# Kernel tuning notes

Measured on AMD Instinct MI355X. Metric: run time of the kernel, lower is better.

Reference implementation:

```python
import jax, jax.numpy as jnp
import numpy as np

N, DIM, H, HD = 2048, 1280, 16, 80

def _rotate_half(x):
    x1, x2 = x[..., :x.shape[-1] // 2], x[..., x.shape[-1] // 2:]
    return jnp.concatenate((-x2, x1), axis=-1)

def setup_inputs() -> dict:
    key = jax.random.key(0)
    ks = jax.random.split(key, 6)
    hidden_states = jax.random.normal(ks[0], (N, DIM), dtype=jnp.float32)
    cu_seqlens = jnp.array([0, N // 2, N], dtype=jnp.int32)  # 2 packed segments
    # rotary embeddings: half-dim inverse frequencies, duplicated to head_dim
    inv_freq = 1.0 / (10000.0 ** (np.arange(0, HD // 2, dtype=np.float32) * 2.0 / HD))
    pos = np.arange(N, dtype=np.float32) % (N // 2)  # positions restart per segment
    freqs = pos[:, None] * inv_freq[None, :]           # [N, HD/2]
    emb = jnp.asarray(np.concatenate([freqs, freqs], axis=-1))  # [N, HD]
    cos, sin = jnp.cos(emb), jnp.sin(emb)
    Wqkv = jax.random.normal(ks[1], (DIM, 3 * DIM), dtype=jnp.float32) * (DIM ** -0.5)
    bqkv = jax.random.normal(ks[2], (3 * DIM,), dtype=jnp.float32) * 0.02
    Wproj = jax.random.normal(ks[3], (DIM, DIM), dtype=jnp.float32) * (DIM ** -0.5)
    bproj = jax.random.normal(ks[4], (DIM,), dtype=jnp.float32) * 0.02
    return {"hidden_states": hidden_states, "cu_seqlens": cu_seqlens,
            "cos": cos, "sin": sin, "Wqkv": Wqkv, "bqkv": bqkv,
            "Wproj": Wproj, "bproj": bproj}

def reference(hidden_states, cu_seqlens, cos, sin, Wqkv, bqkv, Wproj, bproj):
    n = hidden_states.shape[0]
    scale = HD ** -0.5
    qkv = (hidden_states @ Wqkv + bqkv).reshape(n, 3, H, HD)
    q, k, v = qkv[:, 0], qkv[:, 1], qkv[:, 2]           # each [N, H, HD]
    # RoPE (fp32), cos/sin broadcast over heads: [N, 1, HD]
    c, s = cos[:, None, :], sin[:, None, :]
    q = q * c + _rotate_half(q) * s
    k = k * c + _rotate_half(k) * s
    # block-diagonal varlen mask from cu_seqlens (per-segment full attention)
    seg_id = jnp.searchsorted(cu_seqlens, jnp.arange(n), side='right')  # [N]
    mask = seg_id[:, None] == seg_id[None, :]                           # [N, N]
    scores = jnp.einsum('qhd,khd->hqk', q, k) * scale                   # [H, N, N]
    scores = jnp.where(mask[None], scores, -jnp.inf)
    attn = jax.nn.softmax(scores.astype(jnp.float32), axis=-1).astype(q.dtype)
    out = jnp.einsum('hqk,khd->qhd', attn, v).reshape(n, H * HD)        # [N, DIM]
    return out @ Wproj + bproj
```

## Files before the change

### kernel.cpp

```cpp
#include <hip/hip_runtime.h>
#include <hip/hip_bf16.h>

constexpr int N_TOK  = 2048;
constexpr int DIM    = 1280;
constexpr int NHEAD  = 16;
constexpr int HD     = 80;
constexpr int QKV_N  = 3 * DIM;

using bf16 = __hip_bfloat16;
typedef __attribute__((ext_vector_type(4))) float f32x4;
typedef __attribute__((ext_vector_type(8))) short short8;

__device__ __forceinline__ float b2f(bf16 x) { return __bfloat162float(x); }
__device__ __forceinline__ bf16  f2b(float x) { return __float2bfloat16(x); }

typedef const __attribute__((address_space(1))) unsigned int* gas_u32;
typedef __attribute__((address_space(3))) unsigned int* las_u32;
__device__ __forceinline__ void gload_lds16(const void* g, void* l) {
  __builtin_amdgcn_global_load_lds((gas_u32)g, (las_u32)l, 16, 0, 0);
}

__device__ __forceinline__ void transpose_body(const float* __restrict__ W,
                                               bf16* __restrict__ WT, int K, int N) {
  __shared__ float tile[32][33];
  const int n0 = blockIdx.x * 32, k0 = blockIdx.y * 32;
  const int tc = threadIdx.x & 31, tr = threadIdx.x >> 5;
#pragma unroll
  for (int r = tr; r < 32; r += 8)
    tile[r][tc] = W[(size_t)(k0 + r) * N + n0 + tc];
  __syncthreads();
#pragma unroll
  for (int r = tr; r < 32; r += 8)
    WT[(size_t)(n0 + r) * K + k0 + tc] = f2b(tile[tc][r]);
}

__global__ __launch_bounds__(256)
void prep_kernel(const float* __restrict__ hs, bf16* __restrict__ hsb,
                 const float* __restrict__ Wqkv, bf16* __restrict__ WqkvT,
                 const float* __restrict__ Wproj, bf16* __restrict__ WprojT) {
  if (blockIdx.z == 0) {
    const int bid = blockIdx.y * gridDim.x + blockIdx.x;
    if (bid >= (N_TOK * DIM) / 2048) return;
    const int i = bid * 2048 + threadIdx.x * 8;
    const float4 a = *reinterpret_cast<const float4*>(hs + i);
    const float4 b = *reinterpret_cast<const float4*>(hs + i + 4);
    __align__(16) bf16 w[8] = {f2b(a.x), f2b(a.y), f2b(a.z), f2b(a.w),
                               f2b(b.x), f2b(b.y), f2b(b.z), f2b(b.w)};
    *reinterpret_cast<short8*>(hsb + i) = *reinterpret_cast<const short8*>(w);
  } else if (blockIdx.z == 1) {
    transpose_body(Wqkv, WqkvT, DIM, QKV_N);
  } else {
    if (blockIdx.x >= DIM / 32) return;
    transpose_body(Wproj, WprojT, DIM, DIM);
  }
}

template <int OBF>
__global__ __launch_bounds__(256)
void mfma_gemm(const bf16* __restrict__ A, const bf16* __restrict__ BT,
               const float* __restrict__ bias, void* __restrict__ C,
               int M, int N, int K) {
  __shared__ bf16 As[128 * 64];
  __shared__ bf16 Bs[128 * 64];
  const int tid = threadIdx.x;
  const int wid = tid >> 6, lane = tid & 63;
  const int lm = lane & 15, kg = lane >> 4;
  const int wm = (wid >> 1) * 64, wn = (wid & 1) * 64;
  const int m0 = blockIdx.y * 128, n0 = blockIdx.x * 128;

  const int srow = lane >> 3;
  const int sblk = (lane & 7) ^ srow;

  f32x4 acc[4][4];
#pragma unroll
  for (int i = 0; i < 4; ++i)
#pragma unroll
    for (int j = 0; j < 4; ++j) acc[i][j] = (f32x4){0.f, 0.f, 0.f, 0.f};

  for (int k0 = 0; k0 < K; k0 += 64) {
#pragma unroll
    for (int i = 0; i < 4; ++i) {
      const int slot = i * 4 + wid;
      const int row = slot * 8 + srow;
      gload_lds16(A + (size_t)(m0 + row) * K + k0 + sblk * 8, &As[slot * 512]);
      gload_lds16(BT + (size_t)(n0 + row) * K + k0 + sblk * 8, &Bs[slot * 512]);
    }
    __syncthreads();

#pragma unroll
    for (int kh = 0; kh < 2; ++kh) {
      short8 af[4], bfr[4];
#pragma unroll
      for (int t = 0; t < 4; ++t) {
        const int ar = wm + t * 16 + lm;
        af[t] = *reinterpret_cast<const short8*>(
            &As[ar * 64 + ((kh * 4 + kg) ^ (ar & 7)) * 8]);
        const int br = wn + t * 16 + lm;
        bfr[t] = *reinterpret_cast<const short8*>(
            &Bs[br * 64 + ((kh * 4 + kg) ^ (br & 7)) * 8]);
      }
#pragma unroll
      for (int mi = 0; mi < 4; ++mi)
#pragma unroll
        for (int ni = 0; ni < 4; ++ni)
          acc[mi][ni] = __builtin_amdgcn_mfma_f32_16x16x32_bf16(
              af[mi], bfr[ni], acc[mi][ni], 0, 0, 0);
    }
    __syncthreads();
  }

#pragma unroll
  for (int mi = 0; mi < 4; ++mi) {
#pragma unroll
    for (int ni = 0; ni < 4; ++ni) {
      const int col = n0 + wn + ni * 16 + lm;
      const float bv = bias[col];
#pragma unroll
      for (int r = 0; r < 4; ++r) {
        const int row = m0 + wm + mi * 16 + kg * 4 + r;
        const float v = acc[mi][ni][r] + bv;
        if constexpr (OBF)
          ((bf16*)C)[(size_t)row * N + col] = f2b(v);
        else
          ((float*)C)[(size_t)row * N + col] = v;
      }
    }
  }
}

__global__ void rope_kernel(bf16* __restrict__ qkv, const float* __restrict__ cosb,
                            const float* __restrict__ sinb) {
  constexpr int HALF = HD / 2;
  int idx = blockIdx.x * blockDim.x + threadIdx.x;
  int n     = idx / (2 * NHEAD * HALF);
  int rem   = idx % (2 * NHEAD * HALF);
  int which = rem / (NHEAD * HALF);
  int rem2  = rem % (NHEAD * HALF);
  int h     = rem2 / HALF;
  int d     = rem2 % HALF;
  size_t base = (size_t)n * QKV_N + which * DIM + h * HD;
  float x1 = b2f(qkv[base + d]), x2 = b2f(qkv[base + d + HALF]);
  float c1 = cosb[n * HD + d], c2 = cosb[n * HD + d + HALF];
  float s1 = sinb[n * HD + d], s2 = sinb[n * HD + d + HALF];
  qkv[base + d]        = f2b(x1 * c1 - x2 * s1);
  qkv[base + d + HALF] = f2b(x2 * c2 + x1 * s2);
}

constexpr int KC   = 64;
constexpr int KSTR = 104;
constexpr int VSTR = 88;
constexpr int PSTR = 72;

__global__ __launch_bounds__(512)
void attn_mfma_kernel(const bf16* __restrict__ qkv, const int* __restrict__ cu,
                      bf16* __restrict__ out, int nseg) {
  __shared__ bf16 Ks[2][KC * KSTR];
  __shared__ bf16 Vt[HD * VSTR];
  __shared__ bf16 Pl[8 * 16 * PSTR];

  const int p = blockIdx.x;
  const int lidx = (p & 7) * (gridDim.x >> 3) + (p >> 3);
  const int xt  = lidx & 15;
  const int seg = (lidx >> 4) % nseg;
  const int h   = (lidx >> 4) / nseg;

  const int s0 = cu[seg], s1 = cu[seg + 1];
  if (s0 + xt * 128 >= s1) return;

  const int tid  = threadIdx.x;
  const int wid  = tid >> 6, lane = tid & 63;
  const int lm = lane & 15, kg = lane >> 4;
  const int qrow = s0 + xt * 128 + wid * 16 + lm;
  const float scale = 0.11180339887498949f;

  if (tid < 384) {
    int b = tid / 192, rem = tid % 192, r = rem / 3, sl = rem % 3;
    *reinterpret_cast<short8*>(&Ks[b][r * KSTR + 80 + sl * 8]) =
        (short8){0, 0, 0, 0, 0, 0, 0, 0};
  }

  short8 qa[3];
#pragma unroll
  for (int ck = 0; ck < 3; ++ck) {
    const int dbase = ck * 32 + kg * 8;
    if (qrow < s1 && dbase < HD)
      qa[ck] = *reinterpret_cast<const short8*>(
          qkv + (size_t)qrow * QKV_N + h * HD + dbase);
    else
      qa[ck] = (short8){0, 0, 0, 0, 0, 0, 0, 0};
  }

  short8 kreg[2], vreg[4];
  const int vgrp = tid / 10, vsl = tid % 10;
  auto issueK = [&](int c) {
    const int k0 = s0 + c * KC;
    {
      const int r = min(k0 + tid / 10, s1 - 1);
      kreg[0] = *reinterpret_cast<const short8*>(
          qkv + (size_t)r * QKV_N + DIM + h * HD + (tid % 10) * 8);
    }
    if (tid < 128) {
      const int s = tid + 512;
      const int r = min(k0 + s / 10, s1 - 1);
      kreg[1] = *reinterpret_cast<const short8*>(
          qkv + (size_t)r * QKV_N + DIM + h * HD + (s % 10) * 8);
    }
  };
  auto commitK = [&](int buf) {
    *reinterpret_cast<short8*>(&Ks[buf][(tid / 10) * KSTR + (tid % 10) * 8]) =
        kreg[0];
    if (tid < 128) {
      const int s = tid + 512;
      *reinterpret_cast<short8*>(&Ks[buf][(s / 10) * KSTR + (s % 10) * 8]) =
          kreg[1];
    }
  };
  auto issueV = [&](int c) {
    if (tid < 160) {
      const int k0 = s0 + c * KC;
#pragma unroll
      for (int e = 0; e < 4; ++e) {
        const int r = min(k0 + vgrp * 4 + e, s1 - 1);
        vreg[e] = *reinterpret_cast<const short8*>(
            qkv + (size_t)r * QKV_N + 2 * DIM + h * HD + vsl * 8);
      }
    }
  };
  auto commitV = [&]() {
    if (tid < 160) {
      const int r0 = vgrp * 4;
      const int swz = (vsl & 7) << 3;
#pragma unroll
      for (int de = 0; de < 8; ++de) {
        __align__(8) bf16 w[4] = {reinterpret_cast<const bf16*>(&vreg[0])[de],
                                  reinterpret_cast<const bf16*>(&vreg[1])[de],
                                  reinterpret_cast<const bf16*>(&vreg[2])[de],
                                  reinterpret_cast<const bf16*>(&vreg[3])[de]};
        *reinterpret_cast<uint2*>(&Vt[(vsl * 8 + de) * VSTR + (r0 ^ swz)]) =
            *reinterpret_cast<const uint2*>(w);
      }
    }
  };

  f32x4 oacc[5];
#pragma unroll
  for (int dt = 0; dt < 5; ++dt) oacc[dt] = (f32x4){0.f, 0.f, 0.f, 0.f};
  float m = -1e30f, l = 0.f;
  const int plbase = (wid * 16 + lm) * PSTR;
  const int nch = (s1 - s0 + KC - 1) / KC;

  issueK(0);
  issueV(0);
  commitK(0);
  if (nch > 1) issueK(1);
  __syncthreads();

  for (int c = 0; c < nch; ++c) {
    const int cur = c & 1;
    const int nk = min(KC, s1 - (s0 + c * KC));

    commitV();

    f32x4 sc[4];
    __builtin_amdgcn_s_setprio(1);
#pragma unroll
    for (int mi = 0; mi < 4; ++mi) {
      sc[mi] = (f32x4){0.f, 0.f, 0.f, 0.f};
#pragma unroll
      for (int ck = 0; ck < 3; ++ck) {
        short8 ka = *reinterpret_cast<const short8*>(
            &Ks[cur][(mi * 16 + lm) * KSTR + ck * 32 + kg * 8]);
        sc[mi] = __builtin_amdgcn_mfma_f32_16x16x32_bf16(ka, qa[ck], sc[mi], 0, 0, 0);
      }
    }
    __builtin_amdgcn_s_setprio(0);

    if (c + 1 < nch) {
      commitK(cur ^ 1);
      issueV(c + 1);
    }
    if (c + 2 < nch) issueK(c + 2);

#pragma unroll
    for (int mi = 0; mi < 4; ++mi) sc[mi] *= scale;
    if (nk < KC) {
#pragma unroll
      for (int mi = 0; mi < 4; ++mi)
#pragma unroll
        for (int r = 0; r < 4; ++r)
          if (mi * 16 + kg * 4 + r >= nk) sc[mi][r] = -1e30f;
    }
    f32x4 m4 = sc[0];
#pragma unroll
    for (int mi = 1; mi < 4; ++mi) {
      m4[0] = fmaxf(m4[0], sc[mi][0]); m4[1] = fmaxf(m4[1], sc[mi][1]);
      m4[2] = fmaxf(m4[2], sc[mi][2]); m4[3] = fmaxf(m4[3], sc[mi][3]);
    }
    const float rml = fmaxf(fmaxf(m4[0], m4[1]), fmaxf(m4[2], m4[3]));
    if (!__all(rml - m <= 8.0f)) {
      float rm = rml;
      rm = fmaxf(rm, __shfl_xor(rm, 16));
      rm = fmaxf(rm, __shfl_xor(rm, 32));
      const float mnew = fmaxf(m, rm);
      const float fs = __expf(m - mnew);
      m = mnew;
      l *= fs;
#pragma unroll
      for (int dt = 0; dt < 5; ++dt) oacc[dt] *= fs;
    }
    f32x4 pp[4];
#pragma unroll
    for (int mi = 0; mi < 4; ++mi) {
#pragma unroll
      for (int r = 0; r < 4; ++r) {
        pp[mi][r] = __expf(sc[mi][r] - m);
        l += pp[mi][r];
      }
    }
#pragma unroll
    for (int mi = 0; mi < 4; ++mi) {
      __align__(8) bf16 w[4] = {f2b(pp[mi][0]), f2b(pp[mi][1]),
                                f2b(pp[mi][2]), f2b(pp[mi][3])};
      *reinterpret_cast<uint2*>(&Pl[plbase + mi * 16 + kg * 4]) =
          *reinterpret_cast<const uint2*>(w);
    }

    __syncthreads();

    __builtin_amdgcn_s_setprio(1);
#pragma unroll
    for (int kc = 0; kc < 2; ++kc) {
      short8 pb = *reinterpret_cast<const short8*>(&Pl[plbase + kc * 32 + kg * 8]);
#pragma unroll
      for (int dt = 0; dt < 5; ++dt) {
        const int d = dt * 16 + lm;
        short8 va = *reinterpret_cast<const short8*>(
            &Vt[d * VSTR + ((kc * 32 + kg * 8) ^ (((d >> 3) & 7) << 3))]);
        oacc[dt] = __builtin_amdgcn_mfma_f32_16x16x32_bf16(va, pb, oacc[dt], 0, 0, 0);
      }
    }
    __builtin_amdgcn_s_setprio(0);

    __syncthreads();
  }

  l += __shfl_xor(l, 16);
  l += __shfl_xor(l, 32);
  if (qrow < s1) {
    const float inv = 1.f / l;
    bf16* op = out + (size_t)qrow * DIM + h * HD;
#pragma unroll
    for (int dt = 0; dt < 5; ++dt) {
      __align__(8) bf16 w[4] = {f2b(oacc[dt][0] * inv), f2b(oacc[dt][1] * inv),
                                f2b(oacc[dt][2] * inv), f2b(oacc[dt][3] * inv)};
      *reinterpret_cast<uint2*>(op + dt * 16 + kg * 4) =
          *reinterpret_cast<const uint2*>(w);
    }
  }
}

extern "C" void kernel_launch(void* const* d_in, const int* in_sizes, int n_in,
                              void* d_out, int out_size, void* d_ws, size_t ws_size,
                              hipStream_t stream) {
  const float* hs    = (const float*)d_in[0];
  const int*   cu    = (const int*)d_in[1];
  const float* cosb  = (const float*)d_in[2];
  const float* sinb  = (const float*)d_in[3];
  const float* Wqkv  = (const float*)d_in[4];
  const float* bqkv  = (const float*)d_in[5];
  const float* Wproj = (const float*)d_in[6];
  const float* bproj = (const float*)d_in[7];

  bf16* qkv      = (bf16*)d_ws;
  bf16* attn_out = qkv + (size_t)N_TOK * QKV_N;
  bf16* WqkvT    = attn_out + (size_t)N_TOK * DIM;
  bf16* WprojT   = WqkvT + (size_t)QKV_N * DIM;
  bf16* hsb      = WprojT + (size_t)DIM * DIM;

  prep_kernel<<<dim3(QKV_N / 32, DIM / 32, 3), 256, 0, stream>>>(
      hs, hsb, Wqkv, WqkvT, Wproj, WprojT);

  mfma_gemm<1><<<dim3(QKV_N / 128, N_TOK / 128), 256, 0, stream>>>(
      hsb, WqkvT, bqkv, qkv, N_TOK, QKV_N, DIM);

  rope_kernel<<<(N_TOK * 2 * NHEAD * (HD / 2)) / 256, 256, 0, stream>>>(
      qkv, cosb, sinb);

  int nseg = in_sizes[1] - 1;
  int nblk = (N_TOK / 128) * nseg * NHEAD;
  attn_mfma_kernel<<<nblk, 512, 0, stream>>>(qkv, cu, attn_out, nseg);

  mfma_gemm<0><<<dim3(DIM / 128, N_TOK / 128), 256, 0, stream>>>(
      attn_out, WprojT, bproj, d_out, N_TOK, DIM, DIM);
}
```

Baseline: 124.2 us.

## Process two query tiles per wave in attention to reuse K/V LDS fragments

The attention kernel now runs 256 threads (4 waves) per block instead of 512, and each wave handles 32 query rows as two 16-row MFMA tiles. Each K fragment and each V fragment read from LDS feeds two MFMAs, which halves LDS read traffic per unit of math and doubles the independent MFMA work in flight per wave. Online-softmax state (max, sum, output accumulators) is kept separately for each tile, and the K load and LDS padding loops are restructured for the smaller thread count. The cost is higher register pressure from the doubled accumulators, and fewer waves per block, which gives less latency hiding per block.

```diff
diff --git a/kernel.cpp b/kernel.cpp
--- a/kernel.cpp
+++ b/kernel.cpp
@@ -151,12 +151,12 @@
 constexpr int VSTR = 88;
 constexpr int PSTR = 72;
 
-__global__ __launch_bounds__(512)
+__global__ __launch_bounds__(256)
 void attn_mfma_kernel(const bf16* __restrict__ qkv, const int* __restrict__ cu,
                       bf16* __restrict__ out, int nseg) {
   __shared__ bf16 Ks[2][KC * KSTR];
   __shared__ bf16 Vt[HD * VSTR];
-  __shared__ bf16 Pl[8 * 16 * PSTR];
+  __shared__ bf16 Pl[128 * PSTR];
 
   const int p = blockIdx.x;
   const int lidx = (p & 7) * (gridDim.x >> 3) + (p >> 3);
@@ -170,49 +170,54 @@
   const int tid  = threadIdx.x;
   const int wid  = tid >> 6, lane = tid & 63;
   const int lm = lane & 15, kg = lane >> 4;
-  const int qrow = s0 + xt * 128 + wid * 16 + lm;
   const float scale = 0.11180339887498949f;
 
-  if (tid < 384) {
-    int b = tid / 192, rem = tid % 192, r = rem / 3, sl = rem % 3;
-    *reinterpret_cast<short8*>(&Ks[b][r * KSTR + 80 + sl * 8]) =
-        (short8){0, 0, 0, 0, 0, 0, 0, 0};
-  }
-
-  short8 qa[3];
+  const int qbase = s0 + xt * 128 + wid * 32 + lm;
+  const int qrow0 = qbase, qrow1 = qbase + 16;
+
+#pragma unroll
+  for (int t = 0; t < 2; ++t) {
+    const int s = tid + t * 256;
+    if (s < 384) {
+      int b = s / 192, rem = s % 192, r = rem / 3, sl = rem % 3;
+      *reinterpret_cast<short8*>(&Ks[b][r * KSTR + 80 + sl * 8]) =
+          (short8){0, 0, 0, 0, 0, 0, 0, 0};
+    }
+  }
+
+  short8 qa[3][2];
 #pragma unroll
   for (int ck = 0; ck < 3; ++ck) {
     const int dbase = ck * 32 + kg * 8;
-    if (qrow < s1 && dbase < HD)
-      qa[ck] = *reinterpret_cast<const short8*>(
-          qkv + (size_t)qrow * QKV_N + h * HD + dbase);
-    else
-      qa[ck] = (short8){0, 0, 0, 0, 0, 0, 0, 0};
-  }
-
-  short8 kreg[2], vreg[4];
+    qa[ck][0] = (qrow0 < s1 && dbase < HD)
+        ? *reinterpret_cast<const short8*>(qkv + (size_t)qrow0 * QKV_N + h * HD + dbase)
+        : (short8){0, 0, 0, 0, 0, 0, 0, 0};
+    qa[ck][1] = (qrow1 < s1 && dbase < HD)
+        ? *reinterpret_cast<const short8*>(qkv + (size_t)qrow1 * QKV_N + h * HD + dbase)
+        : (short8){0, 0, 0, 0, 0, 0, 0, 0};
+  }
+
+  short8 kreg[3], vreg[4];
   const int vgrp = tid / 10, vsl = tid % 10;
   auto issueK = [&](int c) {
     const int k0 = s0 + c * KC;
-    {
-      const int r = min(k0 + tid / 10, s1 - 1);
-      kreg[0] = *reinterpret_cast<const short8*>(
-          qkv + (size_t)r * QKV_N + DIM + h * HD + (tid % 10) * 8);
-    }
-    if (tid < 128) {
-      const int s = tid + 512;
-      const int r = min(k0 + s / 10, s1 - 1);
-      kreg[1] = *reinterpret_cast<const short8*>(
-          qkv + (size_t)r * QKV_N + DIM + h * HD + (s % 10) * 8);
+#pragma unroll
+    for (int t = 0; t < 3; ++t) {
+      const int s = tid + t * 256;
+      if (s < 640) {
+        const int r = min(k0 + s / 10, s1 - 1);
+        kreg[t] = *reinterpret_cast<const short8*>(
+            qkv + (size_t)r * QKV_N + DIM + h * HD + (s % 10) * 8);
+      }
     }
   };
   auto commitK = [&](int buf) {
-    *reinterpret_cast<short8*>(&Ks[buf][(tid / 10) * KSTR + (tid % 10) * 8]) =
-        kreg[0];
-    if (tid < 128) {
-      const int s = tid + 512;
-      *reinterpret_cast<short8*>(&Ks[buf][(s / 10) * KSTR + (s % 10) * 8]) =
-          kreg[1];
+#pragma unroll
+    for (int t = 0; t < 3; ++t) {
+      const int s = tid + t * 256;
+      if (s < 640)
+        *reinterpret_cast<short8*>(&Ks[buf][(s / 10) * KSTR + (s % 10) * 8]) =
+            kreg[t];
     }
   };
   auto issueV = [&](int c) {
@@ -242,11 +247,16 @@
     }
   };
 
-  f32x4 oacc[5];
-#pragma unroll
-  for (int dt = 0; dt < 5; ++dt) oacc[dt] = (f32x4){0.f, 0.f, 0.f, 0.f};
-  float m = -1e30f, l = 0.f;
-  const int plbase = (wid * 16 + lm) * PSTR;
+  f32x4 oacc[5][2];
+#pragma unroll
+  for (int dt = 0; dt < 5; ++dt) {
+    oacc[dt][0] = (f32x4){0.f, 0.f, 0.f, 0.f};
+    oacc[dt][1] = (f32x4){0.f, 0.f, 0.f, 0.f};
+  }
+  float m0v = -1e30f, m1v = -1e30f;
+  float l0 = 0.f, l1 = 0.f;
+  const int prow0 = (wid * 32 + lm) * PSTR;
+  const int prow1 = (wid * 32 + 16 + lm) * PSTR;
   const int nch = (s1 - s0 + KC - 1) / KC;
 
   issueK(0);
@@ -261,16 +271,20 @@
 
     commitV();
 
-    f32x4 sc[4];
+    f32x4 sc[4][2];
     __builtin_amdgcn_s_setprio(1);
 #pragma unroll
     for (int mi = 0; mi < 4; ++mi) {
-      sc[mi] = (f32x4){0.f, 0.f, 0.f, 0.f};
+      sc[mi][0] = (f32x4){0.f, 0.f, 0.f, 0.f};
+      sc[mi][1] = (f32x4){0.f, 0.f, 0.f, 0.f};
 #pragma unroll
       for (int ck = 0; ck < 3; ++ck) {
         short8 ka = *reinterpret_cast<const short8*>(
             &Ks[cur][(mi * 16 + lm) * KSTR + ck * 32 + kg * 8]);
-        sc[mi] = __builtin_amdgcn_mfma_f32_16x16x32_bf16(ka, qa[ck], sc[mi], 0, 0, 0);
+        sc[mi][0] = __builtin_amdgcn_mfma_f32_16x16x32_bf16(ka, qa[ck][0],
+                                                            sc[mi][0], 0, 0, 0);
+        sc[mi][1] = __builtin_amdgcn_mfma_f32_16x16x32_bf16(ka, qa[ck][1],
+                                                            sc[mi][1], 0, 0, 0);
       }
     }
     __builtin_amdgcn_s_setprio(0);
@@ -282,47 +296,66 @@
     if (c + 2 < nch) issueK(c + 2);
 
 #pragma unroll
-    for (int mi = 0; mi < 4; ++mi) sc[mi] *= scale;
+    for (int mi = 0; mi < 4; ++mi) {
+      sc[mi][0] *= scale;
+      sc[mi][1] *= scale;
+    }
     if (nk < KC) {
 #pragma unroll
       for (int mi = 0; mi < 4; ++mi)
 #pragma unroll
         for (int r = 0; r < 4; ++r)
-          if (mi * 16 + kg * 4 + r >= nk) sc[mi][r] = -1e30f;
-    }
-    f32x4 m4 = sc[0];
-#pragma unroll
-    for (int mi = 1; mi < 4; ++mi) {
-      m4[0] = fmaxf(m4[0], sc[mi][0]); m4[1] = fmaxf(m4[1], sc[mi][1]);
-      m4[2] = fmaxf(m4[2], sc[mi][2]); m4[3] = fmaxf(m4[3], sc[mi][3]);
-    }
-    const float rml = fmaxf(fmaxf(m4[0], m4[1]), fmaxf(m4[2], m4[3]));
-    if (!__all(rml - m <= 8.0f)) {
-      float rm = rml;
-      rm = fmaxf(rm, __shfl_xor(rm, 16));
-      rm = fmaxf(rm, __shfl_xor(rm, 32));
-      const float mnew = fmaxf(m, rm);
-      const float fs = __expf(m - mnew);
-      m = mnew;
-      l *= fs;
-#pragma unroll
-      for (int dt = 0; dt < 5; ++dt) oacc[dt] *= fs;
-    }
-    f32x4 pp[4];
+          if (mi * 16 + kg * 4 + r >= nk) {
+            sc[mi][0][r] = -1e30f;
+            sc[mi][1][r] = -1e30f;
+          }
+    }
+    float rml0 = sc[0][0][0], rml1 = sc[0][1][0];
+#pragma unroll
+    for (int mi = 0; mi < 4; ++mi)
+#pragma unroll
+      for (int r = 0; r < 4; ++r) {
+        if (mi | r) {
+          rml0 = fmaxf(rml0, sc[mi][0][r]);
+          rml1 = fmaxf(rml1, sc[mi][1][r]);
+        }
+      }
+    if (!__all(fmaxf(rml0 - m0v, rml1 - m1v) <= 8.0f)) {
+      float rm0 = rml0, rm1 = rml1;
+      rm0 = fmaxf(rm0, __shfl_xor(rm0, 16));
+      rm0 = fmaxf(rm0, __shfl_xor(rm0, 32));
+      rm1 = fmaxf(rm1, __shfl_xor(rm1, 16));
+      rm1 = fmaxf(rm1, __shfl_xor(rm1, 32));
+      const float mn0 = fmaxf(m0v, rm0), mn1 = fmaxf(m1v, rm1);
+      const float fs0 = __expf(m0v - mn0), fs1 = __expf(m1v - mn1);
+      m0v = mn0; m1v = mn1;
+      l0 *= fs0; l1 *= fs1;
+#pragma unroll
+      for (int dt = 0; dt < 5; ++dt) {
+        oacc[dt][0] *= fs0;
+        oacc[dt][1] *= fs1;
+      }
+    }
 #pragma unroll
     for (int mi = 0; mi < 4; ++mi) {
 #pragma unroll
       for (int r = 0; r < 4; ++r) {
-        pp[mi][r] = __expf(sc[mi][r] - m);
-        l += pp[mi][r];
+        sc[mi][0][r] = __expf(sc[mi][0][r] - m0v);
+        l0 += sc[mi][0][r];
+        sc[mi][1][r] = __expf(sc[mi][1][r] - m1v);
+        l1 += sc[mi][1][r];
       }
     }
 #pragma unroll
     for (int mi = 0; mi < 4; ++mi) {
-      __align__(8) bf16 w[4] = {f2b(pp[mi][0]), f2b(pp[mi][1]),
-                                f2b(pp[mi][2]), f2b(pp[mi][3])};
-      *reinterpret_cast<uint2*>(&Pl[plbase + mi * 16 + kg * 4]) =
-          *reinterpret_cast<const uint2*>(w);
+      __align__(8) bf16 w0[4] = {f2b(sc[mi][0][0]), f2b(sc[mi][0][1]),
+                                 f2b(sc[mi][0][2]), f2b(sc[mi][0][3])};
+      __align__(8) bf16 w1[4] = {f2b(sc[mi][1][0]), f2b(sc[mi][1][1]),
+                                 f2b(sc[mi][1][2]), f2b(sc[mi][1][3])};
+      *reinterpret_cast<uint2*>(&Pl[prow0 + mi * 16 + kg * 4]) =
+          *reinterpret_cast<const uint2*>(w0);
+      *reinterpret_cast<uint2*>(&Pl[prow1 + mi * 16 + kg * 4]) =
+          *reinterpret_cast<const uint2*>(w1);
     }
 
     __syncthreads();
@@ -330,13 +363,17 @@
     __builtin_amdgcn_s_setprio(1);
 #pragma unroll
     for (int kc = 0; kc < 2; ++kc) {
-      short8 pb = *reinterpret_cast<const short8*>(&Pl[plbase + kc * 32 + kg * 8]);
+      short8 pb0 = *reinterpret_cast<const short8*>(&Pl[prow0 + kc * 32 + kg * 8]);
+      short8 pb1 = *reinterpret_cast<const short8*>(&Pl[prow1 + kc * 32 + kg * 8]);
 #pragma unroll
       for (int dt = 0; dt < 5; ++dt) {
         const int d = dt * 16 + lm;
         short8 va = *reinterpret_cast<const short8*>(
             &Vt[d * VSTR + ((kc * 32 + kg * 8) ^ (((d >> 3) & 7) << 3))]);
-        oacc[dt] = __builtin_amdgcn_mfma_f32_16x16x32_bf16(va, pb, oacc[dt], 0, 0, 0);
+        oacc[dt][0] = __builtin_amdgcn_mfma_f32_16x16x32_bf16(va, pb0,
+                                                              oacc[dt][0], 0, 0, 0);
+        oacc[dt][1] = __builtin_amdgcn_mfma_f32_16x16x32_bf16(va, pb1,
+                                                              oacc[dt][1], 0, 0, 0);
       }
     }
     __builtin_amdgcn_s_setprio(0);
@@ -344,15 +381,28 @@
     __syncthreads();
   }
 
-  l += __shfl_xor(l, 16);
-  l += __shfl_xor(l, 32);
-  if (qrow < s1) {
-    const float inv = 1.f / l;
-    bf16* op = out + (size_t)qrow * DIM + h * HD;
+  l0 += __shfl_xor(l0, 16);
+  l0 += __shfl_xor(l0, 32);
+  l1 += __shfl_xor(l1, 16);
+  l1 += __shfl_xor(l1, 32);
+  if (qrow0 < s1) {
+    const float inv = 1.f / l0;
+    bf16* op = out + (size_t)qrow0 * DIM + h * HD;
 #pragma unroll
     for (int dt = 0; dt < 5; ++dt) {
-      __align__(8) bf16 w[4] = {f2b(oacc[dt][0] * inv), f2b(oacc[dt][1] * inv),
-                                f2b(oacc[dt][2] * inv), f2b(oacc[dt][3] * inv)};
+      __align__(8) bf16 w[4] = {f2b(oacc[dt][0][0] * inv), f2b(oacc[dt][0][1] * inv),
+                                f2b(oacc[dt][0][2] * inv), f2b(oacc[dt][0][3] * inv)};
+      *reinterpret_cast<uint2*>(op + dt * 16 + kg * 4) =
+          *reinterpret_cast<const uint2*>(w);
+    }
+  }
+  if (qrow1 < s1) {
+    const float inv = 1.f / l1;
+    bf16* op = out + (size_t)qrow1 * DIM + h * HD;
+#pragma unroll
+    for (int dt = 0; dt < 5; ++dt) {
+      __align__(8) bf16 w[4] = {f2b(oacc[dt][1][0] * inv), f2b(oacc[dt][1][1] * inv),
+                                f2b(oacc[dt][1][2] * inv), f2b(oacc[dt][1][3] * inv)};
       *reinterpret_cast<uint2*>(op + dt * 16 + kg * 4) =
           *reinterpret_cast<const uint2*>(w);
     }
@@ -388,7 +438,7 @@
 
   int nseg = in_sizes[1] - 1;
   int nblk = (N_TOK / 128) * nseg * NHEAD;
-  attn_mfma_kernel<<<nblk, 512, 0, stream>>>(qkv, cu, attn_out, nseg);
+  attn_mfma_kernel<<<nblk, 256, 0, stream>>>(qkv, cu, attn_out, nseg);
 
   mfma_gemm<0><<<dim3(DIM / 128, N_TOK / 128), 256, 0, stream>>>(
       attn_out, WprojT, bproj, d_out, N_TOK, DIM, DIM);
```

Result: faster. 114.3 us (-8.0%).

## Switch attention to 32x32x16 MFMA with register-resident P via permlane32 swap

Applied to the files above, without the earlier changes.

Rewrites the attention kernel to use 32x32x16 bf16 MFMA tiles, so each wave owns 32 query rows and the block shrinks to 4 waves of 256 threads. The softmax probabilities no longer round-trip through the LDS P buffer; they are packed to bf16 and reshuffled across lane halves with permlane32_swap to form the B operand of the PV MFMA directly. V is padded to 96 rows so the head dimension fits three 32-wide tiles. This removes LDS traffic for P and reduces shuffle work, at the cost of wasted MFMA work on the padded head dims and fewer waves per block.

```diff
diff --git a/kernel.cpp b/kernel.cpp
--- a/kernel.cpp
+++ b/kernel.cpp
@@ -8,11 +8,17 @@
 constexpr int QKV_N  = 3 * DIM;
 
 using bf16 = __hip_bfloat16;
-typedef __attribute__((ext_vector_type(4))) float f32x4;
-typedef __attribute__((ext_vector_type(8))) short short8;
+typedef __attribute__((ext_vector_type(4)))  float f32x4;
+typedef __attribute__((ext_vector_type(16))) float f32x16;
+typedef __attribute__((ext_vector_type(8)))  short short8;
 
 __device__ __forceinline__ float b2f(bf16 x) { return __bfloat162float(x); }
 __device__ __forceinline__ bf16  f2b(float x) { return __float2bfloat16(x); }
+
+__device__ __forceinline__ unsigned int pk2(float a, float b) {
+  __align__(4) bf16 t[2] = {f2b(a), f2b(b)};
+  return *reinterpret_cast<unsigned int*>(t);
+}
 
 typedef const __attribute__((address_space(1))) unsigned int* gas_u32;
 typedef __attribute__((address_space(3))) unsigned int* las_u32;
@@ -149,14 +155,13 @@
 constexpr int KC   = 64;
 constexpr int KSTR = 104;
 constexpr int VSTR = 88;
-constexpr int PSTR = 72;
-
-__global__ __launch_bounds__(512)
+constexpr int VROWS = 96;
+
+__global__ __launch_bounds__(256)
 void attn_mfma_kernel(const bf16* __restrict__ qkv, const int* __restrict__ cu,
                       bf16* __restrict__ out, int nseg) {
   __shared__ bf16 Ks[2][KC * KSTR];
-  __shared__ bf16 Vt[HD * VSTR];
-  __shared__ bf16 Pl[8 * 16 * PSTR];
+  __shared__ bf16 Vt[VROWS * VSTR];
 
   const int p = blockIdx.x;
   const int lidx = (p & 7) * (gridDim.x >> 3) + (p >> 3);
@@ -169,50 +174,48 @@
 
   const int tid  = threadIdx.x;
   const int wid  = tid >> 6, lane = tid & 63;
-  const int lm = lane & 15, kg = lane >> 4;
-  const int qrow = s0 + xt * 128 + wid * 16 + lm;
+  const int l31  = lane & 31;
+  const int half = lane >> 5;
   const float scale = 0.11180339887498949f;
 
-  if (tid < 384) {
-    int b = tid / 192, rem = tid % 192, r = rem / 3, sl = rem % 3;
-    *reinterpret_cast<short8*>(&Ks[b][r * KSTR + 80 + sl * 8]) =
+  const int qrow = s0 + xt * 128 + wid * 32 + l31;
+
+  if (tid < 176) {
+    int r = 80 + tid / 11, sl = tid % 11;
+    *reinterpret_cast<short8*>(&Vt[r * VSTR + sl * 8]) =
         (short8){0, 0, 0, 0, 0, 0, 0, 0};
   }
 
-  short8 qa[3];
-#pragma unroll
-  for (int ck = 0; ck < 3; ++ck) {
-    const int dbase = ck * 32 + kg * 8;
-    if (qrow < s1 && dbase < HD)
-      qa[ck] = *reinterpret_cast<const short8*>(
-          qkv + (size_t)qrow * QKV_N + h * HD + dbase);
-    else
-      qa[ck] = (short8){0, 0, 0, 0, 0, 0, 0, 0};
-  }
-
-  short8 kreg[2], vreg[4];
+  short8 qa[5];
+#pragma unroll
+  for (int ck = 0; ck < 5; ++ck) {
+    const int dbase = ck * 16 + half * 8;
+    qa[ck] = (qrow < s1)
+        ? *reinterpret_cast<const short8*>(qkv + (size_t)qrow * QKV_N + h * HD + dbase)
+        : (short8){0, 0, 0, 0, 0, 0, 0, 0};
+  }
+
+  short8 kreg[3], vreg[4];
   const int vgrp = tid / 10, vsl = tid % 10;
   auto issueK = [&](int c) {
     const int k0 = s0 + c * KC;
-    {
-      const int r = min(k0 + tid / 10, s1 - 1);
-      kreg[0] = *reinterpret_cast<const short8*>(
-          qkv + (size_t)r * QKV_N + DIM + h * HD + (tid % 10) * 8);
-    }
-    if (tid < 128) {
-      const int s = tid + 512;
-      const int r = min(k0 + s / 10, s1 - 1);
-      kreg[1] = *reinterpret_cast<const short8*>(
-          qkv + (size_t)r * QKV_N + DIM + h * HD + (s % 10) * 8);
+#pragma unroll
+    for (int t = 0; t < 3; ++t) {
+      const int s = tid + t * 256;
+      if (s < 640) {
+        const int r = min(k0 + s / 10, s1 - 1);
+        kreg[t] = *reinterpret_cast<const short8*>(
+            qkv + (size_t)r * QKV_N + DIM + h * HD + (s % 10) * 8);
+      }
     }
   };
   auto commitK = [&](int buf) {
-    *reinterpret_cast<short8*>(&Ks[buf][(tid / 10) * KSTR + (tid % 10) * 8]) =
-        kreg[0];
-    if (tid < 128) {
-      const int s = tid + 512;
-      *reinterpret_cast<short8*>(&Ks[buf][(s / 10) * KSTR + (s % 10) * 8]) =
-          kreg[1];
+#pragma unroll
+    for (int t = 0; t < 3; ++t) {
+      const int s = tid + t * 256;
+      if (s < 640)
+        *reinterpret_cast<short8*>(&Ks[buf][(s / 10) * KSTR + (s % 10) * 8]) =
+            kreg[t];
     }
   };
   auto issueV = [&](int c) {
@@ -242,11 +245,12 @@
     }
   };
 
-  f32x4 oacc[5];
-#pragma unroll
-  for (int dt = 0; dt < 5; ++dt) oacc[dt] = (f32x4){0.f, 0.f, 0.f, 0.f};
+  f32x16 oacc[3];
+#pragma unroll
+  for (int dt = 0; dt < 3; ++dt)
+#pragma unroll
+    for (int r = 0; r < 16; ++r) oacc[dt][r] = 0.f;
   float m = -1e30f, l = 0.f;
-  const int plbase = (wid * 16 + lm) * PSTR;
   const int nch = (s1 - s0 + KC - 1) / KC;
 
   issueK(0);
@@ -261,16 +265,17 @@
 
     commitV();
 
-    f32x4 sc[4];
+    f32x16 sc[2];
     __builtin_amdgcn_s_setprio(1);
 #pragma unroll
-    for (int mi = 0; mi < 4; ++mi) {
-      sc[mi] = (f32x4){0.f, 0.f, 0.f, 0.f};
-#pragma unroll
-      for (int ck = 0; ck < 3; ++ck) {
+    for (int kt = 0; kt < 2; ++kt) {
+#pragma unroll
+      for (int r = 0; r < 16; ++r) sc[kt][r] = 0.f;
+#pragma unroll
+      for (int ck = 0; ck < 5; ++ck) {
         short8 ka = *reinterpret_cast<const short8*>(
-            &Ks[cur][(mi * 16 + lm) * KSTR + ck * 32 + kg * 8]);
-        sc[mi] = __builtin_amdgcn_mfma_f32_16x16x32_bf16(ka, qa[ck], sc[mi], 0, 0, 0);
+            &Ks[cur][(kt * 32 + l31) * KSTR + ck * 16 + half * 8]);
+        sc[kt] = __builtin_amdgcn_mfma_f32_32x32x16_bf16(ka, qa[ck], sc[kt], 0, 0, 0);
       }
     }
     __builtin_amdgcn_s_setprio(0);
@@ -282,61 +287,74 @@
     if (c + 2 < nch) issueK(c + 2);
 
 #pragma unroll
-    for (int mi = 0; mi < 4; ++mi) sc[mi] *= scale;
+    for (int kt = 0; kt < 2; ++kt)
+#pragma unroll
+      for (int r = 0; r < 16; ++r) sc[kt][r] *= scale;
     if (nk < KC) {
 #pragma unroll
-      for (int mi = 0; mi < 4; ++mi)
-#pragma unroll
-        for (int r = 0; r < 4; ++r)
-          if (mi * 16 + kg * 4 + r >= nk) sc[mi][r] = -1e30f;
-    }
-    f32x4 m4 = sc[0];
-#pragma unroll
-    for (int mi = 1; mi < 4; ++mi) {
-      m4[0] = fmaxf(m4[0], sc[mi][0]); m4[1] = fmaxf(m4[1], sc[mi][1]);
-      m4[2] = fmaxf(m4[2], sc[mi][2]); m4[3] = fmaxf(m4[3], sc[mi][3]);
-    }
-    const float rml = fmaxf(fmaxf(m4[0], m4[1]), fmaxf(m4[2], m4[3]));
+      for (int kt = 0; kt < 2; ++kt)
+#pragma unroll
+        for (int r = 0; r < 16; ++r) {
+          const int key = kt * 32 + (r & 3) + 8 * (r >> 2) + 4 * half;
+          if (key >= nk) sc[kt][r] = -1e30f;
+        }
+    }
+    float rml = sc[0][0];
+#pragma unroll
+    for (int kt = 0; kt < 2; ++kt)
+#pragma unroll
+      for (int r = 0; r < 16; ++r)
+        if (kt | r) rml = fmaxf(rml, sc[kt][r]);
     if (!__all(rml - m <= 8.0f)) {
-      float rm = rml;
-      rm = fmaxf(rm, __shfl_xor(rm, 16));
-      rm = fmaxf(rm, __shfl_xor(rm, 32));
+      float rm = fmaxf(rml, __shfl_xor(rml, 32));
       const float mnew = fmaxf(m, rm);
       const float fs = __expf(m - mnew);
       m = mnew;
       l *= fs;
 #pragma unroll
-      for (int dt = 0; dt < 5; ++dt) oacc[dt] *= fs;
-    }
-    f32x4 pp[4];
-#pragma unroll
-    for (int mi = 0; mi < 4; ++mi) {
-#pragma unroll
-      for (int r = 0; r < 4; ++r) {
-        pp[mi][r] = __expf(sc[mi][r] - m);
-        l += pp[mi][r];
-      }
-    }
-#pragma unroll
-    for (int mi = 0; mi < 4; ++mi) {
-      __align__(8) bf16 w[4] = {f2b(pp[mi][0]), f2b(pp[mi][1]),
-                                f2b(pp[mi][2]), f2b(pp[mi][3])};
-      *reinterpret_cast<uint2*>(&Pl[plbase + mi * 16 + kg * 4]) =
-          *reinterpret_cast<const uint2*>(w);
+      for (int dt = 0; dt < 3; ++dt)
+#pragma unroll
+        for (int r = 0; r < 16; ++r) oacc[dt][r] *= fs;
+    }
+#pragma unroll
+    for (int kt = 0; kt < 2; ++kt)
+#pragma unroll
+      for (int r = 0; r < 16; ++r) {
+        sc[kt][r] = __expf(sc[kt][r] - m);
+        l += sc[kt][r];
+      }
+
+    unsigned int pbw[4][4];
+#pragma unroll
+    for (int kt = 0; kt < 2; ++kt) {
+      unsigned int w[8];
+#pragma unroll
+      for (int i = 0; i < 8; ++i) w[i] = pk2(sc[kt][2 * i], sc[kt][2 * i + 1]);
+#pragma unroll
+      for (int kc2 = 0; kc2 < 2; ++kc2) {
+        auto r02 = __builtin_amdgcn_permlane32_swap(w[4 * kc2 + 0],
+                                                    w[4 * kc2 + 2], false, false);
+        auto r13 = __builtin_amdgcn_permlane32_swap(w[4 * kc2 + 1],
+                                                    w[4 * kc2 + 3], false, false);
+        pbw[kt * 2 + kc2][0] = r02[0];
+        pbw[kt * 2 + kc2][1] = r13[0];
+        pbw[kt * 2 + kc2][2] = r02[1];
+        pbw[kt * 2 + kc2][3] = r13[1];
+      }
     }
 
     __syncthreads();
 
     __builtin_amdgcn_s_setprio(1);
 #pragma unroll
-    for (int kc = 0; kc < 2; ++kc) {
-      short8 pb = *reinterpret_cast<const short8*>(&Pl[plbase + kc * 32 + kg * 8]);
-#pragma unroll
-      for (int dt = 0; dt < 5; ++dt) {
-        const int d = dt * 16 + lm;
+    for (int kc = 0; kc < 4; ++kc) {
+      short8 pb = *reinterpret_cast<const short8*>(&pbw[kc][0]);
+#pragma unroll
+      for (int dt = 0; dt < 3; ++dt) {
+        const int d = dt * 32 + l31;
         short8 va = *reinterpret_cast<const short8*>(
-            &Vt[d * VSTR + ((kc * 32 + kg * 8) ^ (((d >> 3) & 7) << 3))]);
-        oacc[dt] = __builtin_amdgcn_mfma_f32_16x16x32_bf16(va, pb, oacc[dt], 0, 0, 0);
+            &Vt[d * VSTR + ((kc * 16 + half * 8) ^ (((d >> 3) & 7) << 3))]);
+        oacc[dt] = __builtin_amdgcn_mfma_f32_32x32x16_bf16(va, pb, oacc[dt], 0, 0, 0);
       }
     }
     __builtin_amdgcn_s_setprio(0);
@@ -344,17 +362,23 @@
     __syncthreads();
   }
 
-  l += __shfl_xor(l, 16);
   l += __shfl_xor(l, 32);
   if (qrow < s1) {
     const float inv = 1.f / l;
     bf16* op = out + (size_t)qrow * DIM + h * HD;
 #pragma unroll
-    for (int dt = 0; dt < 5; ++dt) {
-      __align__(8) bf16 w[4] = {f2b(oacc[dt][0] * inv), f2b(oacc[dt][1] * inv),
-                                f2b(oacc[dt][2] * inv), f2b(oacc[dt][3] * inv)};
-      *reinterpret_cast<uint2*>(op + dt * 16 + kg * 4) =
-          *reinterpret_cast<const uint2*>(w);
+    for (int dt = 0; dt < 3; ++dt) {
+#pragma unroll
+      for (int g = 0; g < 4; ++g) {
+        const int d = dt * 32 + g * 8 + half * 4;
+        if (d < HD) {
+          __align__(8) bf16 w[4] = {f2b(oacc[dt][g * 4 + 0] * inv),
+                                    f2b(oacc[dt][g * 4 + 1] * inv),
+                                    f2b(oacc[dt][g * 4 + 2] * inv),
+                                    f2b(oacc[dt][g * 4 + 3] * inv)};
+          *reinterpret_cast<uint2*>(op + d) = *reinterpret_cast<const uint2*>(w);
+        }
+      }
     }
   }
 }
@@ -388,7 +412,7 @@
 
   int nseg = in_sizes[1] - 1;
   int nblk = (N_TOK / 128) * nseg * NHEAD;
-  attn_mfma_kernel<<<nblk, 512, 0, stream>>>(qkv, cu, attn_out, nseg);
+  attn_mfma_kernel<<<nblk, 256, 0, stream>>>(qkv, cu, attn_out, nseg);
 
   mfma_gemm<0><<<dim3(DIM / 128, N_TOK / 128), 256, 0, stream>>>(
       attn_out, WprojT, bproj, d_out, N_TOK, DIM, DIM);
```

New measurement: 113.8 us. -8.4%, faster.
